# Optimization experiments

Hardware: AMD Instinct MI355X
Metric: run time of the kernel (lower is better)

The kernel has to match this reference:

```python
import jax, jax.numpy as jnp
import numpy as np

B, T, NN = 128, 128, 8          # batch, time_window, nodes per graph (hardcoded in source)
N = B * T * NN                  # 131072 flattened node rows
F_IN, C = 32, 64                # node_features, spatial_features
E = 1_048_576                   # edges (avg degree 8)
EPS = 1e-5


def _gcn(x, src, dst, W, b):
    # PyG GCNConv: h = D^{-1/2}(A+I)D^{-1/2} X W + b, self-loops added, symmetric norm
    h = x @ W                                           # [N, C]
    loop = jnp.arange(N, dtype=src.dtype)
    s = jnp.concatenate([src, loop])
    d = jnp.concatenate([dst, loop])
    deg = jax.ops.segment_sum(jnp.ones_like(s, dtype=h.dtype), d, num_segments=N)
    dinv = jax.lax.rsqrt(deg)                           # deg >= 1 due to self loops
    msg = h[s] * (dinv[s] * dinv[d])[:, None]           # gather + scale
    out = jax.ops.segment_sum(msg, d, num_segments=N)   # scatter-add
    return out + b


def _conv2d(x, w, b, pad_w):
    y = jax.lax.conv_general_dilated(
        x, w, window_strides=(1, 1), padding=[(0, 0), (pad_w, pad_w)],
        dimension_numbers=("NCHW", "OIHW", "NCHW"))
    return y + b[None, :, None, None]


def _bn_relu(x, g, beta):
    # BatchNorm2d in training mode: batch statistics, biased variance
    mu = x.mean(axis=(0, 2, 3), keepdims=True)
    var = x.var(axis=(0, 2, 3), keepdims=True)
    y = (x - mu) * jax.lax.rsqrt(var + EPS)
    return jax.nn.relu(y * g[None, :, None, None] + beta[None, :, None, None])


def _layer(x, src, dst, gw, gb, tw, tb, bg, bb, ow, ob):
    h = _gcn(x, src, dst, gw, gb)                       # [N, C]
    h = h.reshape(B, T, NN, -1).transpose(0, 3, 2, 1)   # [B, C, NN, T]
    h = _conv2d(h, tw, tb, 1)                           # (1,3) temporal conv, pad (0,1)
    h = _bn_relu(h, bg, bb)
    h = _conv2d(h, ow, ob, 0)                           # 1x1 conv (squeeze() is a no-op here)
    h = jnp.tanh(h)
    return h.reshape(-1, h.shape[1])                    # faithful to x.view(-1, x.shape[1])


def setup_inputs() -> dict:
    key = jax.random.key(0)
    ks = jax.random.split(key, 20)
    p = lambda k, shape: (jax.random.normal(k, shape, jnp.float32) * 0.05)
    inp = {
        "x": jax.random.normal(ks[0], (N, F_IN), jnp.float32),
        "edge_index": jax.random.randint(ks[1], (2, E), 0, N, jnp.int32),
        "gcn1_w": p(ks[2], (F_IN, C)), "gcn1_b": jnp.zeros((C,), jnp.float32),
        "t1_w": p(ks[3], (C, C, 1, 3)), "t1_b": jnp.zeros((C,), jnp.float32),
        "bn1_g": jnp.ones((C,), jnp.float32), "bn1_b": jnp.zeros((C,), jnp.float32),
        "o1_w": p(ks[4], (C, C, 1, 1)), "o1_b": jnp.zeros((C,), jnp.float32),
        "gcn2_w": p(ks[5], (C, C)), "gcn2_b": jnp.zeros((C,), jnp.float32),
        "t2_w": p(ks[6], (C, C, 1, 3)), "t2_b": jnp.zeros((C,), jnp.float32),
        "bn2_g": jnp.ones((C,), jnp.float32), "bn2_b": jnp.zeros((C,), jnp.float32),
        "o2_w": p(ks[7], (C, C, 1, 1)), "o2_b": jnp.zeros((C,), jnp.float32),
        "reg_w": p(ks[8], (C, 8)), "reg_b": jnp.zeros((8,), jnp.float32),
    }
    return inp


def reference(x, edge_index, gcn1_w, gcn1_b, t1_w, t1_b, bn1_g, bn1_b, o1_w, o1_b,
              gcn2_w, gcn2_b, t2_w, t2_b, bn2_g, bn2_b, o2_w, o2_b, reg_w, reg_b):
    src, dst = edge_index[0], edge_index[1]
    h = _layer(x, src, dst, gcn1_w, gcn1_b, t1_w, t1_b, bn1_g, bn1_b, o1_w, o1_b)
    h = _layer(h, src, dst, gcn2_w, gcn2_b, t2_w, t2_b, bn2_g, bn2_b, o2_w, o2_b)
    h = h @ reg_w + reg_b                                # [N, 8]
    h = h.reshape(B, T, NN, -1)
    return h.mean(axis=(1, 3))                           # [B, NN] = [128, 8]
```

## Files before the change

kernel.cpp:

```cpp
#include <hip/hip_runtime.h>
#include <stdint.h>

typedef unsigned short u16;
typedef __attribute__((ext_vector_type(8))) short bf16x8;
typedef __attribute__((ext_vector_type(4))) float f32x4;

static const int N_NODES = 131072;
static const int N_EDGES = 1048576;

__device__ __forceinline__ float u2f(u16 u){
  union{uint32_t i; float f;} w; w.i = ((uint32_t)u)<<16; return w.f;
}
__device__ __forceinline__ u16 f2u(float f){
  union{float f; uint32_t u;} v; v.f=f;
  uint32_t u=v.u;
  u += 0x7fff + ((u>>16)&1);
  return (u16)(u>>16);
}
__device__ __forceinline__ float bits2f(uint32_t b){
  union{uint32_t i; float f;} w; w.i = b; return w.f;
}
__device__ __forceinline__ float ldmix(const void* p, int i, int isbf){
  return isbf ? u2f(((const u16*)p)[i]) : ((const float*)p)[i];
}
__device__ __forceinline__ float ftanh(float x){
  float ax = fabsf(x);
  float e  = __expf(ax + ax);
  float r  = 1.f - __fdividef(2.f, e + 1.f);
  return copysignf(r, x);
}

__global__ __launch_bounds__(256) void k_hist(const int* __restrict__ dst, int* __restrict__ H,
                                              const uint32_t* __restrict__ x, int* __restrict__ flag,
                                              float* __restrict__ stats1, float* __restrict__ stats2,
                                              float* __restrict__ zacc){
  __shared__ int h[256];
  __shared__ int dcnt;
  int tid = threadIdx.x;
  h[tid] = 0;
  if (blockIdx.x == 0){
    if (tid == 0) dcnt = 0;
    for (int i=tid; i<512; i+=256){ stats1[i] = 0.f; stats2[i] = 0.f; }
    for (int i=tid; i<1024; i+=256) zacc[i] = 0.f;
  }
  __syncthreads();
  if (blockIdx.x == 0){
    uint32_t e = (x[tid]>>7) & 0xFFu;
    int ok = (e >= 0x6Fu && e <= 0x85u) ? 1 : 0;
    unsigned long long m = __ballot(ok);
    if ((tid & 63) == 0) atomicAdd(&dcnt, (int)__popcll(m));
    __syncthreads();
    if (tid == 0) *flag = (dcnt >= 128) ? 1 : 0;
  }
  int base = blockIdx.x*4096;
  #pragma unroll
  for (int i=0;i<16;i++){
    int e2 = base + i*256 + tid;
    atomicAdd(&h[(dst[e2] & (N_NODES-1))>>9], 1);
  }
  __syncthreads();
  H[blockIdx.x*256 + tid] = h[tid];
}

__device__ __forceinline__ void wcomb_one(int Kin, const void* gW, const void* gb, const void* tw,
                                          int isbf, u16* Wtb, float* braw, int r, int co){
  if (r < 3*Kin){
    int k = r / Kin, j = r - (r/Kin)*Kin;
    float acc = 0.f;
    for (int c=0; c<64; c++)
      acc += ldmix(gW, j*64+c, isbf) * ldmix(tw, co*192 + c*3 + k, isbf);
    Wtb[co*(3*Kin) + r] = f2u(acc);
  } else {
    int k = r - 3*Kin;
    float acc = 0.f;
    for (int c=0; c<64; c++)
      acc += ldmix(gb, c, isbf) * ldmix(tw, co*192 + c*3 + k, isbf);
    braw[k*64 + co] = acc;
  }
}

__global__ __launch_bounds__(256) void k_colscan_w(const int* __restrict__ H, int* __restrict__ P,
                                                   int* __restrict__ bt,
                                                   const void* __restrict__ g1w, const void* __restrict__ g1b,
                                                   const void* __restrict__ t1w,
                                                   const void* __restrict__ g2w, const void* __restrict__ g2b,
                                                   const void* __restrict__ t2w,
                                                   const void* __restrict__ o1w, const void* __restrict__ o2w,
                                                   const int* __restrict__ flag,
                                                   u16* __restrict__ Wtb1, float* __restrict__ braw1,
                                                   u16* __restrict__ Wtb2, float* __restrict__ braw2,
                                                   u16* __restrict__ owb1, u16* __restrict__ owb2){
  int tid = threadIdx.x;
  if (blockIdx.x < 256){
    __shared__ int sc[256];
    int b = blockIdx.x;
    int v = H[tid*256 + b];
    sc[tid] = v; __syncthreads();
    for (int d=1; d<256; d<<=1){
      int o = (tid>=d) ? sc[tid-d] : 0; __syncthreads();
      sc[tid] += o; __syncthreads();
    }
    P[tid*256 + b] = sc[tid] - v;
    if (tid==255) bt[b] = sc[255];
  } else {
    int isbf = *flag;
    int r = (blockIdx.x - 256)*4 + (tid>>6);
    int co = tid & 63;
    if (r >= 422) return;
    if (r < 99) wcomb_one(32, g1w, g1b, t1w, isbf, Wtb1, braw1, r, co);
    else if (r < 294) wcomb_one(64, g2w, g2b, t2w, isbf, Wtb2, braw2, r-99, co);
    else if (r < 358){
      int row = r - 294;
      owb1[row*64 + co] = f2u(ldmix(o1w, row*64 + co, isbf));
    } else {
      int row = r - 358;
      owb2[row*64 + co] = f2u(ldmix(o2w, row*64 + co, isbf));
    }
  }
}

__global__ __launch_bounds__(256) void k_scatter2(const int* __restrict__ src, const int* __restrict__ dst,
                                                  const int* __restrict__ P, const int* __restrict__ bt,
                                                  uint32_t* __restrict__ ebuf){
  __shared__ int cu[256], sc[256];
  int tid = threadIdx.x;
  int v = bt[tid];
  sc[tid] = v; __syncthreads();
  for (int d=1; d<256; d<<=1){
    int o = (tid>=d) ? sc[tid-d] : 0; __syncthreads();
    sc[tid] += o; __syncthreads();
  }
  cu[tid] = (sc[tid] - v) + P[blockIdx.x*256 + tid];
  __syncthreads();
  int base = blockIdx.x*4096;
  #pragma unroll
  for (int i=0;i<16;i++){
    int e = base + i*256 + tid;
    int s = src[e] & (N_NODES-1);
    int d = dst[e] & (N_NODES-1);
    int pos = atomicAdd(&cu[d>>9], 1);
    ebuf[pos] = (uint32_t)s | ((uint32_t)(d & 511) << 17);
  }
}

__global__ __launch_bounds__(512) void k_bsort2(const uint32_t* __restrict__ ebuf, const int* __restrict__ bt,
                                                const void* __restrict__ x, const int* __restrict__ flag,
                                                int* __restrict__ adj, int* __restrict__ offs,
                                                int* __restrict__ deg, float* __restrict__ dinv,
                                                u16* __restrict__ Bout){
  __shared__ uint32_t ein[5120], outs[5120];
  __shared__ int hist[512], sc[512], cu[512];
  __shared__ int sct[256];
  __shared__ float dv[512];
  int b = blockIdx.x, tid = threadIdx.x;
  if (tid < 256){ sct[tid] = bt[tid]; }
  __syncthreads();
  for (int d=1; d<256; d<<=1){
    int o = (tid < 256 && tid>=d) ? sct[tid-d] : 0; __syncthreads();
    if (tid < 256) sct[tid] += o; __syncthreads();
  }
  int lo = sct[b] - bt[b], hi = sct[b];
  int cnt = hi - lo; if (cnt > 5120) cnt = 5120; if (cnt < 0) cnt = 0;
  hist[tid] = 0;
  __syncthreads();
  for (int i=tid; i<cnt; i+=512){
    uint32_t p = ebuf[lo+i];
    ein[i] = p;
    atomicAdd(&hist[(p>>17)&511], 1);
  }
  __syncthreads();
  sc[tid] = hist[tid];
  __syncthreads();
  for (int d=1; d<512; d<<=1){
    int v = (tid>=d) ? sc[tid-d] : 0;
    __syncthreads();
    sc[tid] += v;
    __syncthreads();
  }
  {
    int ex = sc[tid] - hist[tid];
    int node = b*512 + tid;
    offs[node] = lo + ex;
    deg[node]  = hist[tid];
    float rs = rsqrtf((float)hist[tid] + 1.0f);
    dinv[node] = rs;
    dv[tid] = rs;
    cu[tid] = ex;
  }
  __syncthreads();
  for (int i=tid; i<cnt; i+=512){
    uint32_t p = ein[i];
    int pos = atomicAdd(&cu[(p>>17)&511], 1);
    outs[pos] = p & 0x1FFFFu;
  }
  __syncthreads();
  for (int i=tid; i<cnt; i+=512) adj[lo+i] = (int)outs[i];
  int isbf = *flag;
  {
    uint32_t* Bd = (uint32_t*)Bout;
    for (int u=tid; u<8192; u+=512){
      int nl = u>>4, jd = u&15;
      int half = ((b<<9) + nl)*16 + jd;
      float x0, x1;
      if (isbf){
        uint32_t pr = ((const uint32_t*)x)[half];
        x0 = bits2f(pr<<16); x1 = bits2f(pr & 0xFFFF0000u);
      } else {
        float2 f2 = ((const float2*)x)[half];
        x0 = f2.x; x1 = f2.y;
      }
      float d = dv[nl];
      Bd[half] = (uint32_t)f2u(x0*d) | ((uint32_t)f2u(x1*d) << 16);
    }
  }
}

__device__ __forceinline__ void acc16(uint4 a, float* acc){
  acc[0] += bits2f(a.x<<16); acc[1] += bits2f(a.x&0xFFFF0000u);
  acc[2] += bits2f(a.y<<16); acc[3] += bits2f(a.y&0xFFFF0000u);
  acc[4] += bits2f(a.z<<16); acc[5] += bits2f(a.z&0xFFFF0000u);
  acc[6] += bits2f(a.w<<16); acc[7] += bits2f(a.w&0xFFFF0000u);
}

template<int Kin>
__global__ __launch_bounds__(256) void k_gconv(
    const u16* __restrict__ Xs, const int* __restrict__ adj, const int* __restrict__ offs,
    const int* __restrict__ deg, const float* __restrict__ dinv,
    const u16* __restrict__ Wtb, const float* __restrict__ braw, const void* __restrict__ tb,
    const int* __restrict__ flag, u16* __restrict__ out, float* __restrict__ stats){
  constexpr int K   = 3*Kin;
  constexpr int SA  = Kin + 8;
  constexpr int CH  = Kin/8;
  constexpr int GPW = 64/CH;
  __shared__ alignas(16) u16 At[66*SA];
  __shared__ float ball[64], bs0[64], bs2[64];
  __shared__ float wsum[4][64], wsum2[4][64];

  int isbf = *flag;
  int bid = blockIdx.x;
  int b = bid>>4, rem = bid&15, v = rem>>1, th = rem&1;
  const int tid = threadIdx.x;
  int wv_ = tid >> 6, lane = tid & 63;
  int q = lane >> 4, l16 = lane & 15;
  int ltb0 = wv_ * 16;
  int g = lane / CH, kch = lane % CH;
  const uint4* X4 = (const uint4*)Xs;

  if (tid < 64){
    float b0=braw[tid], b1=braw[64+tid], b2=braw[128+tid];
    ball[tid] = ldmix(tb, tid, isbf) + b0 + b1 + b2;
    bs0[tid] = b0; bs2[tid] = b2;
  }

  for (int row = wv_*GPW + g; row < 66; row += 4*GPW){
    int t = th*64 + row - 1;
    uint4 rv = {0,0,0,0};
    if (t >= 0 && t < 128){
      int n = (b*128 + t)*8 + v;
      int o = offs[n] & (N_EDGES-1);
      int cnt = min(deg[n], 8192);
      float dvv = dinv[n];
      float acc[8] = {0,0,0,0,0,0,0,0};
      acc16(X4[(size_t)n*CH + kch], acc);
      {
        int idx[16];
        #pragma unroll
        for (int j=0; j<16; j++){
          int ao = o + j; ao = (ao > N_EDGES-1) ? (N_EDGES-1) : ao;
          int ai = adj[ao] & (N_NODES-1);
          idx[j] = (j < cnt) ? ai : n;
        }
        uint4 av[16];
        #pragma unroll
        for (int j=0; j<16; j++) av[j] = X4[(size_t)idx[j]*CH + kch];
        #pragma unroll
        for (int j=0; j<16; j++){
          uint4 tv = av[j];
          bool act = (j < cnt);
          tv.x = act ? tv.x : 0u; tv.y = act ? tv.y : 0u;
          tv.z = act ? tv.z : 0u; tv.w = act ? tv.w : 0u;
          acc16(tv, acc);
        }
      }
      int e = (cnt < 16) ? cnt : 16;
      for (; e+8 <= cnt; e += 8){
        int i0 = adj[o+e+0] & (N_NODES-1);
        int i1 = adj[o+e+1] & (N_NODES-1);
        int i2 = adj[o+e+2] & (N_NODES-1);
        int i3 = adj[o+e+3] & (N_NODES-1);
        int i4 = adj[o+e+4] & (N_NODES-1);
        int i5 = adj[o+e+5] & (N_NODES-1);
        int i6 = adj[o+e+6] & (N_NODES-1);
        int i7 = adj[o+e+7] & (N_NODES-1);
        uint4 a0 = X4[(size_t)i0*CH + kch];
        uint4 a1 = X4[(size_t)i1*CH + kch];
        uint4 a2 = X4[(size_t)i2*CH + kch];
        uint4 a3 = X4[(size_t)i3*CH + kch];
        uint4 a4 = X4[(size_t)i4*CH + kch];
        uint4 a5 = X4[(size_t)i5*CH + kch];
        uint4 a6 = X4[(size_t)i6*CH + kch];
        uint4 a7 = X4[(size_t)i7*CH + kch];
        acc16(a0, acc); acc16(a1, acc); acc16(a2, acc); acc16(a3, acc);
        acc16(a4, acc); acc16(a5, acc); acc16(a6, acc); acc16(a7, acc);
      }
      if (e+4 <= cnt){
        int i0 = adj[o+e+0] & (N_NODES-1);
        int i1 = adj[o+e+1] & (N_NODES-1);
        int i2 = adj[o+e+2] & (N_NODES-1);
        int i3 = adj[o+e+3] & (N_NODES-1);
        uint4 a0 = X4[(size_t)i0*CH + kch];
        uint4 a1 = X4[(size_t)i1*CH + kch];
        uint4 a2 = X4[(size_t)i2*CH + kch];
        uint4 a3 = X4[(size_t)i3*CH + kch];
        acc16(a0, acc); acc16(a1, acc); acc16(a2, acc); acc16(a3, acc);
        e += 4;
      }
      for (; e < cnt; e++){
        int s = adj[o+e] & (N_NODES-1);
        uint4 a = X4[(size_t)s*CH + kch];
        acc16(a, acc);
      }
      rv.x = (uint32_t)f2u(acc[0]*dvv) | ((uint32_t)f2u(acc[1]*dvv) << 16);
      rv.y = (uint32_t)f2u(acc[2]*dvv) | ((uint32_t)f2u(acc[3]*dvv) << 16);
      rv.z = (uint32_t)f2u(acc[4]*dvv) | ((uint32_t)f2u(acc[5]*dvv) << 16);
      rv.w = (uint32_t)f2u(acc[6]*dvv) | ((uint32_t)f2u(acc[7]*dvv) << 16);
    }
    *(uint4*)&At[row*SA + kch*8] = rv;
  }
  __syncthreads();

  f32x4 acc4[4];
  #pragma unroll
  for (int nt=0; nt<4; nt++) acc4[nt] = (f32x4){0.f,0.f,0.f,0.f};
  #pragma unroll
  for (int s=0; s<K/32; s++){
    int kk2 = (32*s)/Kin;
    int j0 = 32*s - kk2*Kin;
    int col = j0 + q*8;
    bf16x8 afr = *(const bf16x8*)&At[(ltb0 + l16 + kk2)*SA + col];
    bf16x8 bfr[4];
    #pragma unroll
    for (int nt=0; nt<4; nt++){
      int co = nt*16 + l16;
      bfr[nt] = *(const bf16x8*)&Wtb[co*K + 32*s + q*8];
    }
    #pragma unroll
    for (int nt=0; nt<4; nt++)
      acc4[nt] = __builtin_amdgcn_mfma_f32_16x16x32_bf16(afr, bfr[nt], acc4[nt], 0, 0, 0);
  }

  float ls_[4] = {0,0,0,0}, ls2_[4] = {0,0,0,0};
  #pragma unroll
  for (int r=0; r<4; r++){
    int t = th*64 + ltb0 + q*4 + r;
    int base = (((b*128+t)*8+v)) << 6;
    #pragma unroll
    for (int nt=0; nt<4; nt++){
      int co = nt*16 + l16;
      float val = acc4[nt][r] + ball[co];
      if (t == 0)   val -= bs0[co];
      if (t == 127) val -= bs2[co];
      out[base + co] = f2u(val);
      ls_[nt] += val; ls2_[nt] += val*val;
    }
  }
  #pragma unroll
  for (int nt=0; nt<4; nt++){
    ls_[nt]  += __shfl_xor(ls_[nt], 16);  ls_[nt]  += __shfl_xor(ls_[nt], 32);
    ls2_[nt] += __shfl_xor(ls2_[nt], 16); ls2_[nt] += __shfl_xor(ls2_[nt], 32);
  }
  if (q == 0){
    #pragma unroll
    for (int nt=0; nt<4; nt++){
      wsum[wv_][nt*16 + l16]  = ls_[nt];
      wsum2[wv_][nt*16 + l16] = ls2_[nt];
    }
  }
  __syncthreads();
  if (tid < 64){
    float a = wsum[0][tid]+wsum[1][tid]+wsum[2][tid]+wsum[3][tid];
    float a2 = wsum2[0][tid]+wsum2[1][tid]+wsum2[2][tid]+wsum2[3][tid];
    int bank = (bid & 3) * 128;
    atomicAdd(&stats[bank + tid], a);
    atomicAdd(&stats[bank + 64 + tid], a2);
  }
}

template<bool FINAL>
__global__ __launch_bounds__(256) void k_bnfuse3(const u16* __restrict__ X, const float* __restrict__ stats,
                                                 const void* __restrict__ gam, const void* __restrict__ bet,
                                                 const u16* __restrict__ owb, const void* __restrict__ ob,
                                                 const int* __restrict__ flag, const float* __restrict__ presc,
                                                 u16* __restrict__ out16,
                                                 float* __restrict__ zacc, const void* __restrict__ rw){
  constexpr int SA = 72;
  __shared__ alignas(16) u16 Yl[64*SA];
  __shared__ float kk[64], bsh[64], obs[64];
  __shared__ float rw_s[64];
  __shared__ float wred[4];
  int isbf = *flag;
  int bid = blockIdx.x;
  int b = bid>>4, rem = bid&15, v = rem>>1, th = rem&1;
  const int tid = threadIdx.x;
  const float invM = 1.0f/131072.0f;

  if (tid < 64){
    int ci = tid;
    float s1 = stats[ci] + stats[128+ci] + stats[256+ci] + stats[384+ci];
    float s2 = stats[64+ci] + stats[192+ci] + stats[320+ci] + stats[448+ci];
    float mu = s1*invM;
    float var = s2*invM - mu*mu;
    float rs = rsqrtf(fmaxf(var, 0.f) + 1e-5f);
    float kv = rs*ldmix(gam, ci, isbf);
    kk[ci] = kv;
    bsh[ci] = ldmix(bet, ci, isbf) - mu*kv;
    obs[ci] = ldmix(ob, ci, isbf);
    if (FINAL){
      float s = 0.f;
      #pragma unroll
      for (int f=0; f<8; f++) s += ldmix(rw, ci*8 + f, isbf);
      rw_s[ci] = s;
    }
  }
  __syncthreads();
  {
    uint32_t* Yd = (uint32_t*)Yl;
    const uint32_t* Xg = (const uint32_t*)X;
    for (int u=tid; u<64*32; u+=256){
      int lt = u>>5, jd = u&31;
      int ci = jd<<1;
      int t = th*64 + lt;
      int rowbase = (((b*128+t)*8+v)) << 6;
      uint32_t pr = Xg[(rowbase>>1) + jd];
      float x0 = bits2f(pr<<16);
      float x1 = bits2f(pr & 0xFFFF0000u);
      float y0 = fmaxf(x0*kk[ci] + bsh[ci], 0.f);
      float y1 = fmaxf(x1*kk[ci+1] + bsh[ci+1], 0.f);
      Yd[lt*(SA/2) + jd] = (uint32_t)f2u(y0) | ((uint32_t)f2u(y1) << 16);
    }
  }
  __syncthreads();

  int wv_ = tid >> 6, lane = tid & 63;
  int q = lane >> 4, l16 = lane & 15;
  int ltb0 = wv_ * 16;

  f32x4 acc[4];
  #pragma unroll
  for (int nt=0; nt<4; nt++) acc[nt] = (f32x4){0.f,0.f,0.f,0.f};

  #pragma unroll
  for (int s=0; s<2; s++){
    int col = 32*s + q*8;
    bf16x8 afr = *(const bf16x8*)&Yl[(ltb0 + l16)*SA + col];
    bf16x8 bfr[4];
    #pragma unroll
    for (int nt=0; nt<4; nt++){
      int co = nt*16 + l16;
      bfr[nt] = *(const bf16x8*)&owb[co*64 + col];
    }
    #pragma unroll
    for (int nt=0; nt<4; nt++)
      acc[nt] = __builtin_amdgcn_mfma_f32_16x16x32_bf16(afr, bfr[nt], acc[nt], 0, 0, 0);
  }

  __syncthreads();
  #pragma unroll
  for (int r=0; r<4; r++){
    int lt = ltb0 + q*4 + r;
    #pragma unroll
    for (int nt=0; nt<4; nt++){
      int co = nt*16 + l16;
      Yl[lt*SA + co] = f2u(acc[nt][r] + obs[co]);
    }
  }
  __syncthreads();
  if (!FINAL){
    for (int u=tid; u<4096; u+=256){
      int l = u & 63;
      int co = u >> 6;
      float z = ftanh(u2f(Yl[l*SA + co]));
      int r = (b<<10) + (co<<4) + (v<<1) + th;
      if (presc) z *= presc[r];
      out16[(r<<6) + l] = f2u(z);
    }
  } else {
    float zsum = 0.f;
    for (int u=tid; u<4096; u+=256){
      int l = u & 63;
      int co = u >> 6;
      float z = ftanh(u2f(Yl[l*SA + co]));
      zsum += z * rw_s[l];
    }
    for (int off=32; off; off>>=1) zsum += __shfl_down(zsum, off);
    if (lane == 0) wred[wv_] = zsum;
    __syncthreads();
    if (tid == 0){
      int base = (b<<3) + ((v&3)<<1) + th;
      atomicAdd(&zacc[base], wred[0] + wred[1] + wred[2] + wred[3]);
    }
  }
}

__global__ __launch_bounds__(256) void k_fin2(const float* __restrict__ zacc, const void* __restrict__ rb,
                                              const int* __restrict__ flag, void* __restrict__ out){
  int i = blockIdx.x*256 + threadIdx.x;
  if (i >= 1024) return;
  int isbf = *flag;
  float rbs = 0.f;
  #pragma unroll
  for (int f=0; f<8; f++) rbs += ldmix(rb, f, isbf);
  float val = zacc[i]*(1.0f/1024.0f) + rbs*0.125f;
  if (isbf) ((u16*)out)[i] = f2u(val);
  else      ((float*)out)[i] = val;
}

extern "C" void kernel_launch(void* const* d_in, const int* in_sizes, int n_in,
                              void* d_out, int out_size, void* d_ws, size_t ws_size,
                              hipStream_t stream){
  (void)in_sizes; (void)n_in; (void)out_size; (void)ws_size;
  char* p = (char*)d_ws;
  auto alloc = [&](size_t bytes){ void* r = (void*)p; p += (bytes + 255) & ~(size_t)255; return r; };
  u16*   U1   = (u16*)  alloc(sizeof(u16)*(size_t)N_NODES*64);
  u16*   U2   = (u16*)  alloc(sizeof(u16)*(size_t)N_NODES*64);
  u16*   C16  = (u16*)  alloc(sizeof(u16)*(size_t)N_NODES*64);
  int*   deg  = (int*)  alloc(sizeof(int)*N_NODES);
  float* dinv = (float*)alloc(sizeof(float)*N_NODES);
  int*   offs = (int*)  alloc(sizeof(int)*N_NODES);
  int*   adj  = (int*)  alloc(sizeof(int)*N_EDGES);
  int*   H    = (int*)  alloc(sizeof(int)*256*256);
  int*   P    = (int*)  alloc(sizeof(int)*256*256);
  int*   bt   = (int*)  alloc(sizeof(int)*256);
  float* stats1=(float*)alloc(sizeof(float)*512);
  float* stats2=(float*)alloc(sizeof(float)*512);
  int*   flag = (int*)  alloc(sizeof(int)*64);
  u16*   Wtb1 = (u16*)  alloc(sizeof(u16)*96*64);
  float* braw1= (float*)alloc(sizeof(float)*192);
  u16*   Wtb2 = (u16*)  alloc(sizeof(u16)*192*64);
  float* braw2= (float*)alloc(sizeof(float)*192);
  u16*   owb1 = (u16*)  alloc(sizeof(u16)*64*64);
  u16*   owb2 = (u16*)  alloc(sizeof(u16)*64*64);
  float* zacc = (float*)alloc(sizeof(float)*1024);
  uint32_t* ebuf = (uint32_t*)C16;
  u16* Bs16 = U1;
  u16* D16  = U1;
  (void)U2;

  const void* x   = d_in[0];
  const int* edge = (const int*)d_in[1];
  const void* g1w = d_in[2];  const void* g1b = d_in[3];
  const void* t1w = d_in[4];  const void* t1b = d_in[5];
  const void* bn1g= d_in[6];  const void* bn1b= d_in[7];
  const void* o1w = d_in[8];  const void* o1b = d_in[9];
  const void* g2w = d_in[10]; const void* g2b = d_in[11];
  const void* t2w = d_in[12]; const void* t2b = d_in[13];
  const void* bn2g= d_in[14]; const void* bn2b= d_in[15];
  const void* o2w = d_in[16]; const void* o2b = d_in[17];
  const void* rw  = d_in[18]; const void* rb  = d_in[19];
  const int* src = edge;
  const int* dst = edge + N_EDGES;

  k_hist     <<<256, 256, 0, stream>>>(dst, H, (const uint32_t*)x, flag, stats1, stats2, zacc);
  k_colscan_w<<<362, 256, 0, stream>>>(H, P, bt, g1w, g1b, t1w, g2w, g2b, t2w, o1w, o2w, flag,
                                       Wtb1, braw1, Wtb2, braw2, owb1, owb2);
  k_scatter2 <<<256, 256, 0, stream>>>(src, dst, P, bt, ebuf);
  k_bsort2   <<<256, 512, 0, stream>>>(ebuf, bt, x, flag, adj, offs, deg, dinv, Bs16);

  k_gconv<32> <<<2048, 256, 0, stream>>>(Bs16, adj, offs, deg, dinv, Wtb1, braw1, t1b, flag, C16, stats1);
  k_bnfuse3<false><<<2048, 256, 0, stream>>>(C16, stats1, bn1g, bn1b, owb1, o1b, flag, dinv, D16,
                                             (float*)nullptr, (const void*)nullptr);

  k_gconv<64> <<<2048, 256, 0, stream>>>(D16, adj, offs, deg, dinv, Wtb2, braw2, t2b, flag, C16, stats2);
  k_bnfuse3<true><<<2048, 256, 0, stream>>>(C16, stats2, bn2g, bn2b, owb2, o2b, flag, (const float*)nullptr,
                                            (u16*)nullptr, zacc, rw);
  k_fin2<<<4, 256, 0, stream>>>(zacc, rb, flag, d_out);
}
```

Measured before the change: 266.2 us.

## Stage adjacency prefix in LDS and fold final reduction into last bnfuse block

In the graph-conv kernel, the first 16 adjacency indices of each of the 66 rows are now loaded cooperatively into shared memory before the gather loop, so lanes no longer issue redundant scattered adj loads per channel chunk. The final small kernel that turned the accumulated sums into the output is removed; instead the last block of the final bnfuse kernel, detected with a completion counter plus thread fences, writes the output. This saves one launch and some redundant global loads, in exchange for an extra barrier, extra LDS use, and an atomic counter at the end of each block.

```diff
diff --git a/kernel.cpp b/kernel.cpp
--- a/kernel.cpp
+++ b/kernel.cpp
@@ -39,7 +39,7 @@
   int tid = threadIdx.x;
   h[tid] = 0;
   if (blockIdx.x == 0){
-    if (tid == 0) dcnt = 0;
+    if (tid == 0){ dcnt = 0; flag[16] = 0; }
     for (int i=tid; i<512; i+=256){ stats1[i] = 0.f; stats2[i] = 0.f; }
     for (int i=tid; i<1024; i+=256) zacc[i] = 0.f;
   }
@@ -233,6 +233,7 @@
   constexpr int CH  = Kin/8;
   constexpr int GPW = 64/CH;
   __shared__ alignas(16) u16 At[66*SA];
+  __shared__ int adjc[66*16];
   __shared__ float ball[64], bs0[64], bs2[64];
   __shared__ float wsum[4][64], wsum2[4][64];
 
@@ -251,6 +252,20 @@
     ball[tid] = ldmix(tb, tid, isbf) + b0 + b1 + b2;
     bs0[tid] = b0; bs2[tid] = b2;
   }
+
+  for (int u = tid; u < 66*16; u += 256){
+    int row = u >> 4, j = u & 15;
+    int t = th*64 + row - 1;
+    int a = 0;
+    if (t >= 0 && t < 128){
+      int n = (b*128 + t)*8 + v;
+      int o = offs[n] & (N_EDGES-1);
+      int ao = o + j; ao = (ao > N_EDGES-1) ? (N_EDGES-1) : ao;
+      a = adj[ao];
+    }
+    adjc[u] = a;
+  }
+  __syncthreads();
 
   for (int row = wv_*GPW + g; row < 66; row += 4*GPW){
     int t = th*64 + row - 1;
@@ -266,8 +281,7 @@
         int idx[16];
         #pragma unroll
         for (int j=0; j<16; j++){
-          int ao = o + j; ao = (ao > N_EDGES-1) ? (N_EDGES-1) : ao;
-          int ai = adj[ao] & (N_NODES-1);
+          int ai = adjc[(row<<4) + j] & (N_NODES-1);
           idx[j] = (j < cnt) ? ai : n;
         }
         uint4 av[16];
@@ -392,12 +406,15 @@
                                                  const u16* __restrict__ owb, const void* __restrict__ ob,
                                                  const int* __restrict__ flag, const float* __restrict__ presc,
                                                  u16* __restrict__ out16,
-                                                 float* __restrict__ zacc, const void* __restrict__ rw){
+                                                 float* __restrict__ zacc, const void* __restrict__ rw,
+                                                 const void* __restrict__ rb, void* __restrict__ dout,
+                                                 int* __restrict__ dcnt){
   constexpr int SA = 72;
   __shared__ alignas(16) u16 Yl[64*SA];
   __shared__ float kk[64], bsh[64], obs[64];
   __shared__ float rw_s[64];
   __shared__ float wred[4];
+  __shared__ int islast;
   int isbf = *flag;
   int bid = blockIdx.x;
   int b = bid>>4, rem = bid&15, v = rem>>1, th = rem&1;
@@ -498,21 +515,23 @@
     if (tid == 0){
       int base = (b<<3) + ((v&3)<<1) + th;
       atomicAdd(&zacc[base], wred[0] + wred[1] + wred[2] + wred[3]);
-    }
-  }
-}
-
-__global__ __launch_bounds__(256) void k_fin2(const float* __restrict__ zacc, const void* __restrict__ rb,
-                                              const int* __restrict__ flag, void* __restrict__ out){
-  int i = blockIdx.x*256 + threadIdx.x;
-  if (i >= 1024) return;
-  int isbf = *flag;
-  float rbs = 0.f;
-  #pragma unroll
-  for (int f=0; f<8; f++) rbs += ldmix(rb, f, isbf);
-  float val = zacc[i]*(1.0f/1024.0f) + rbs*0.125f;
-  if (isbf) ((u16*)out)[i] = f2u(val);
-  else      ((float*)out)[i] = val;
+      __threadfence();
+      int d = atomicAdd(dcnt, 1);
+      islast = (d == 2047) ? 1 : 0;
+    }
+    __syncthreads();
+    if (islast){
+      __threadfence();
+      float rbs = 0.f;
+      #pragma unroll
+      for (int f=0; f<8; f++) rbs += ldmix(rb, f, isbf);
+      for (int i = tid; i < 1024; i += 256){
+        float val = zacc[i]*(1.0f/1024.0f) + rbs*0.125f;
+        if (isbf) ((u16*)dout)[i] = f2u(val);
+        else      ((float*)dout)[i] = val;
+      }
+    }
+  }
 }
 
 extern "C" void kernel_launch(void* const* d_in, const int* in_sizes, int n_in,
@@ -522,7 +541,6 @@
   char* p = (char*)d_ws;
   auto alloc = [&](size_t bytes){ void* r = (void*)p; p += (bytes + 255) & ~(size_t)255; return r; };
   u16*   U1   = (u16*)  alloc(sizeof(u16)*(size_t)N_NODES*64);
-  u16*   U2   = (u16*)  alloc(sizeof(u16)*(size_t)N_NODES*64);
   u16*   C16  = (u16*)  alloc(sizeof(u16)*(size_t)N_NODES*64);
   int*   deg  = (int*)  alloc(sizeof(int)*N_NODES);
   float* dinv = (float*)alloc(sizeof(float)*N_NODES);
@@ -544,7 +562,6 @@
   uint32_t* ebuf = (uint32_t*)C16;
   u16* Bs16 = U1;
   u16* D16  = U1;
-  (void)U2;
 
   const void* x   = d_in[0];
   const int* edge = (const int*)d_in[1];
@@ -568,10 +585,10 @@
 
   k_gconv<32> <<<2048, 256, 0, stream>>>(Bs16, adj, offs, deg, dinv, Wtb1, braw1, t1b, flag, C16, stats1);
   k_bnfuse3<false><<<2048, 256, 0, stream>>>(C16, stats1, bn1g, bn1b, owb1, o1b, flag, dinv, D16,
-                                             (float*)nullptr, (const void*)nullptr);
+                                             (float*)nullptr, (const void*)nullptr,
+                                             (const void*)nullptr, (void*)nullptr, (int*)nullptr);
 
   k_gconv<64> <<<2048, 256, 0, stream>>>(D16, adj, offs, deg, dinv, Wtb2, braw2, t2b, flag, C16, stats2);
   k_bnfuse3<true><<<2048, 256, 0, stream>>>(C16, stats2, bn2g, bn2b, owb2, o2b, flag, (const float*)nullptr,
-                                            (u16*)nullptr, zacc, rw);
-  k_fin2<<<4, 256, 0, stream>>>(zacc, rb, flag, d_out);
-}
+                                            (u16*)nullptr, zacc, rw, rb, d_out, flag + 16);
+}
```

After: 297.0 us. 1.12x slower.
